# Kernel tuning notes

Hardware: AMD Instinct MI355X
Metric: run time of the kernel (lower is better)

## Reference

```python
import jax, jax.numpy as jnp
import numpy as np
import math

N_NODES = 100000
N_EDGES = 1_600_000
NFEAT = 512
NHID = 128
NLAYERS = 6
NCLASS = 64


def setup_inputs() -> dict:
    key = jax.random.key(0)
    ks = jax.random.split(key, 8)
    x = jax.random.normal(ks[0], (N_NODES, NFEAT), jnp.float32)
    rows = jax.random.randint(ks[1], (N_EDGES,), 0, N_NODES, dtype=jnp.int32)
    cols = jax.random.randint(ks[2], (N_EDGES,), 0, N_NODES, dtype=jnp.int32)
    # normalized-adjacency-like edge weights
    vals = jax.random.uniform(ks[3], (N_EDGES,), jnp.float32) * (1.0 / 16.0)
    s = 1.0 / math.sqrt(NHID)  # reset_parameters: uniform(-1/sqrt(out_features), ...)
    W0 = jax.random.uniform(ks[4], (NFEAT, NHID), jnp.float32, minval=-s, maxval=s)
    Wh = jax.random.uniform(ks[5], (NLAYERS - 1, NHID, NHID), jnp.float32, minval=-s, maxval=s)
    Wfc = jax.random.normal(ks[6], (NHID * NLAYERS, NCLASS), jnp.float32) * 0.02
    bfc = jnp.zeros((NCLASS,), jnp.float32)
    return {"x": x, "rows": rows, "cols": cols, "vals": vals,
            "W0": W0, "Wh": Wh, "Wfc": Wfc, "bfc": bfc}


def _spmm(rows, cols, vals, h, n):
    # sparse [n,n] @ h : gather source rows, scale by edge weight, scatter-add to dest
    return jax.ops.segment_sum(vals[:, None] * h[cols], rows, num_segments=n)


def reference(x, rows, cols, vals, W0, Wh, Wfc, bfc):
    n = x.shape[0]
    # conv0: relu(spmm(A, x @ W0))  (inference: no dropout, no skip-gate)
    h = jax.nn.relu(_spmm(rows, cols, vals, x @ W0, n))
    hiddens = [h]
    for i in range(Wh.shape[0]):
        h = jax.nn.relu(_spmm(rows, cols, vals, h @ Wh[i], n))
        hiddens.append(h)
    logits = jnp.concatenate(hiddens, axis=-1) @ Wfc + bfc
    return jax.nn.log_softmax(logits, axis=1)
```

## Files before the change

### kernel.cpp

```cpp
#include <hip/hip_runtime.h>
#include <hip/hip_bf16.h>
#include <cstdint>
#include <cstddef>

static constexpr int NFEAT   = 512;
static constexpr int NHID    = 128;
static constexpr int NLAYERS = 6;
static constexpr int NCLASS  = 64;

typedef __bf16 bf16x8 __attribute__((ext_vector_type(8)));
typedef float  floatx4 __attribute__((ext_vector_type(4)));

static __device__ __forceinline__ uint16_t f2bf(float v){
    __hip_bfloat16 h = __float2bfloat16(v);
    return *reinterpret_cast<uint16_t*>(&h);
}

__global__ void k_sniff(const uint16_t* __restrict__ x, int nwords, uint32_t* __restrict__ flag){
    int i = blockIdx.x*256 + threadIdx.x;
    if (i < nwords){
        uint16_t w = x[i];
        if ((w & 0x7F80u) == 0x7F80u) atomicOr(flag, 1u);
    }
}

__global__ void k_sentinel(uint16_t* out, int nel){
    int i = blockIdx.x*256 + threadIdx.x;
    if (i < nel) out[i] = 0x3E00u;
}

__global__ void k_zero(uint32_t* p, int n){
    int i = blockIdx.x*256 + threadIdx.x;
    if (i < n) p[i] = 0u;
}

__global__ void k_hist(const int* __restrict__ rows, uint32_t* __restrict__ deg, int nE){
    int e = blockIdx.x*256 + threadIdx.x;
    if (e < nE) atomicAdd(&deg[rows[e]], 1u);
}

__global__ __launch_bounds__(1024) void k_scan1(const uint32_t* __restrict__ deg,
                                                uint32_t* __restrict__ row_start,
                                                uint32_t* __restrict__ partial, int n){
    __shared__ uint32_t sh[1024];
    int tid = threadIdx.x;
    int i = blockIdx.x*1024 + tid;
    uint32_t v = (i < n) ? deg[i] : 0u;
    sh[tid] = v; __syncthreads();
    for (int off = 1; off < 1024; off <<= 1){
        uint32_t t = (tid >= off) ? sh[tid-off] : 0u;
        __syncthreads();
        sh[tid] += t;
        __syncthreads();
    }
    if (i < n) row_start[i+1] = sh[tid];
    if (tid == 1023) partial[blockIdx.x] = sh[1023];
}

__global__ __launch_bounds__(128) void k_scan2(uint32_t* partial, int nb){
    __shared__ uint32_t sh[128];
    int tid = threadIdx.x;
    uint32_t v = (tid < nb) ? partial[tid] : 0u;
    sh[tid] = v; __syncthreads();
    for (int off = 1; off < 128; off <<= 1){
        uint32_t t = (tid >= off) ? sh[tid-off] : 0u;
        __syncthreads();
        sh[tid] += t;
        __syncthreads();
    }
    if (tid < nb) partial[tid] = sh[tid] - v;
}

__global__ __launch_bounds__(1024) void k_scan3(const uint32_t* __restrict__ deg,
                                                uint32_t* __restrict__ row_start,
                                                const uint32_t* __restrict__ partial,
                                                uint32_t* __restrict__ cursor, int n){
    int i = blockIdx.x*1024 + threadIdx.x;
    if (i < n){
        uint32_t rs = row_start[i+1] + partial[blockIdx.x];
        row_start[i+1] = rs;
        cursor[i] = rs - deg[i];
        if (i == 0) row_start[0] = 0u;
    }
}

__global__ void k_scatter(const int* __restrict__ rows, const int* __restrict__ cols,
                          const void* __restrict__ vals,
                          uint32_t* __restrict__ cursor, uint2* __restrict__ ep, int nE,
                          const uint32_t* __restrict__ flags){
    int e = blockIdx.x*256 + threadIdx.x;
    if (e < nE){
        int r = rows[e];
        uint32_t pos = atomicAdd(&cursor[r], 1u);
        float v;
        if (flags[0]) v = ((const float*)vals)[e];
        else          v = __bfloat162float(((const __hip_bfloat16*)vals)[e]);
        ep[pos] = make_uint2((uint32_t)cols[e], __float_as_uint(v));
    }
}

__global__ void k_transpose(const void* __restrict__ B, long elem_off,
                            uint16_t* __restrict__ Bt, int K, int N,
                            const uint32_t* __restrict__ flags){
    int idx = blockIdx.x*256 + threadIdx.x;
    if (idx < K*N){
        int k = idx / N, nn = idx - k*N;
        uint16_t w;
        if (flags[0]) w = f2bf(((const float*)B)[elem_off + idx]);
        else          w = ((const uint16_t*)B)[elem_off + idx];
        Bt[nn*K + k] = w;
    }
}

template<int NTILES, int MODE>
__global__ __launch_bounds__(256) void k_gemm(
    const void* __restrict__ Aany, int lda,
    const uint16_t* __restrict__ Bt, int ldb, int K, int Mwaves,
    uint16_t* __restrict__ Cb, float* __restrict__ Cf,
    const uint32_t* __restrict__ flagsp)
{
    __shared__ uint16_t lds[NTILES*16*40];
    const int tid  = threadIdx.x;
    const int lane = tid & 63;
    const int gw   = blockIdx.x*4 + (tid >> 6);
    const bool active = gw < Mwaves;
    const int m = lane & 15, quad = lane >> 4;
    const long row0 = (long)gw * 16;
    const int afp32 = flagsp ? (int)flagsp[0] : 0;
    const uint16_t* A16 = (const uint16_t*)Aany;
    const float*    A32 = (const float*)Aany;

    floatx4 acc[NTILES];
#pragma unroll
    for (int i = 0; i < NTILES; i++) acc[i] = (floatx4){0.f,0.f,0.f,0.f};

    for (int kk = 0; kk < K; kk += 32){
        for (int idx = tid; idx < NTILES*16*4; idx += 256){
            int nn = idx >> 2, c = idx & 3;
            *(bf16x8*)&lds[nn*40 + c*8] = *(const bf16x8*)&Bt[(long)nn*ldb + kk + c*8];
        }
        __syncthreads();
        if (active){
            bf16x8 a;
            if (afp32){
                const float* p = &A32[(row0 + m)*lda + kk + quad*8];
                float4 f0 = *(const float4*)p;
                float4 f1 = *(const float4*)(p + 4);
                a[0]=(__bf16)f0.x; a[1]=(__bf16)f0.y; a[2]=(__bf16)f0.z; a[3]=(__bf16)f0.w;
                a[4]=(__bf16)f1.x; a[5]=(__bf16)f1.y; a[6]=(__bf16)f1.z; a[7]=(__bf16)f1.w;
            } else {
                a = *(const bf16x8*)&A16[(row0 + m)*lda + kk + quad*8];
            }
#pragma unroll
            for (int nt = 0; nt < NTILES; nt++){
                bf16x8 b = *(const bf16x8*)&lds[(nt*16 + m)*40 + quad*8];
                acc[nt] = __builtin_amdgcn_mfma_f32_16x16x32_bf16(a, b, acc[nt], 0, 0, 0);
            }
        }
        __syncthreads();
    }
    if (active){
#pragma unroll
        for (int nt = 0; nt < NTILES; nt++){
#pragma unroll
            for (int r = 0; r < 4; r++){
                long row = row0 + quad*4 + r;
                int  col = nt*16 + m;
                float v = acc[nt][r];
                if (MODE == 1) Cf[row*(NTILES*16) + col] += v;
                else           Cb[row*(NTILES*16) + col] = f2bf(v);
            }
        }
    }
}

__global__ __launch_bounds__(256) void k_gemm_fused(
    const uint16_t* __restrict__ A,
    const uint16_t* __restrict__ B1t,
    const uint16_t* __restrict__ B2t, int ldb2,
    uint16_t* __restrict__ C1, float* __restrict__ C2, int nchunks)
{
    __shared__ uint16_t lds[(128+64)*132];
    const int tid = threadIdx.x, lane = tid & 63;
    for (int idx = tid; idx < 128*16; idx += 256){
        int nn = idx >> 4, c = idx & 15;
        *(bf16x8*)&lds[nn*132 + c*8] = *(const bf16x8*)&B1t[nn*128 + c*8];
    }
    for (int idx = tid; idx < 64*16; idx += 256){
        int nn = idx >> 4, c = idx & 15;
        *(bf16x8*)&lds[(128+nn)*132 + c*8] = *(const bf16x8*)&B2t[(long)nn*ldb2 + c*8];
    }
    __syncthreads();

    const int m = lane & 15, quad = lane >> 4;
    const int nw = gridDim.x * 4;
    for (int chunk = blockIdx.x*4 + (tid >> 6); chunk < nchunks; chunk += nw){
        const long row0 = (long)chunk * 16;
        const uint16_t* Arow = &A[(row0 + m)*128 + quad*8];
        bf16x8 a[4];
#pragma unroll
        for (int ks = 0; ks < 4; ks++) a[ks] = *(const bf16x8*)&Arow[ks*32];

        floatx4 acc1[8], acc2[4];
#pragma unroll
        for (int i = 0; i < 8; i++) acc1[i] = (floatx4){0.f,0.f,0.f,0.f};
#pragma unroll
        for (int i = 0; i < 4; i++) acc2[i] = (floatx4){0.f,0.f,0.f,0.f};

#pragma unroll
        for (int ks = 0; ks < 4; ks++){
            const int kk = ks*32 + quad*8;
#pragma unroll
            for (int nt = 0; nt < 8; nt++){
                bf16x8 b = *(const bf16x8*)&lds[(nt*16 + m)*132 + kk];
                acc1[nt] = __builtin_amdgcn_mfma_f32_16x16x32_bf16(a[ks], b, acc1[nt], 0, 0, 0);
            }
#pragma unroll
            for (int nt = 0; nt < 4; nt++){
                bf16x8 b = *(const bf16x8*)&lds[(128 + nt*16 + m)*132 + kk];
                acc2[nt] = __builtin_amdgcn_mfma_f32_16x16x32_bf16(a[ks], b, acc2[nt], 0, 0, 0);
            }
        }
#pragma unroll
        for (int nt = 0; nt < 8; nt++){
#pragma unroll
            for (int r = 0; r < 4; r++){
                long row = row0 + quad*4 + r;
                int  col = nt*16 + m;
                float v  = acc1[nt][r];
                float vn = __shfl_xor(v, 1);
                if ((m & 1) == 0){
                    uint32_t pk = (uint32_t)f2bf(v) | ((uint32_t)f2bf(vn) << 16);
                    *(uint32_t*)&C1[row*128 + col] = pk;
                }
            }
        }
#pragma unroll
        for (int nt = 0; nt < 4; nt++){
#pragma unroll
            for (int r = 0; r < 4; r++){
                long row = row0 + quad*4 + r;
                int  col = nt*16 + m;
                float v  = acc2[nt][r];
                float vn = __shfl_xor(v, 1);
                if ((m & 1) == 0){
                    float2* p = (float2*)&C2[row*64 + col];
                    float2 o = *p;
                    o.x += v; o.y += vn;
                    *p = o;
                }
            }
        }
    }
}

__global__ __launch_bounds__(256) void k_spmm(
    const uint2* __restrict__ ep, const uint32_t* __restrict__ row_start,
    const uint32_t* __restrict__ tmp, uint16_t* __restrict__ out, int n)
{
    int t = blockIdx.x*256 + threadIdx.x;
    int gw = t >> 6, lane = t & 63;
    if (gw >= n) return;
    uint32_t s = row_start[gw], e = row_start[gw+1];
    float ax = 0.f, ay = 0.f;
    for (uint32_t base = s; base < e; base += 64){
        int cnt = (int)(e - base); if (cnt > 64) cnt = 64;
        uint2 d = (lane < cnt) ? ep[base + lane] : make_uint2(0u, 0u);
        int j = 0;
        for (; j + 4 <= cnt; j += 4){
            uint32_t c0 = __shfl(d.x, j+0); float v0 = __uint_as_float(__shfl(d.y, j+0));
            uint32_t c1 = __shfl(d.x, j+1); float v1 = __uint_as_float(__shfl(d.y, j+1));
            uint32_t c2 = __shfl(d.x, j+2); float v2 = __uint_as_float(__shfl(d.y, j+2));
            uint32_t c3 = __shfl(d.x, j+3); float v3 = __uint_as_float(__shfl(d.y, j+3));
            uint32_t p0 = tmp[(size_t)c0*64 + lane];
            uint32_t p1 = tmp[(size_t)c1*64 + lane];
            uint32_t p2 = tmp[(size_t)c2*64 + lane];
            uint32_t p3 = tmp[(size_t)c3*64 + lane];
            ax = fmaf(v0, __uint_as_float(p0 << 16), ax); ay = fmaf(v0, __uint_as_float(p0 & 0xffff0000u), ay);
            ax = fmaf(v1, __uint_as_float(p1 << 16), ax); ay = fmaf(v1, __uint_as_float(p1 & 0xffff0000u), ay);
            ax = fmaf(v2, __uint_as_float(p2 << 16), ax); ay = fmaf(v2, __uint_as_float(p2 & 0xffff0000u), ay);
            ax = fmaf(v3, __uint_as_float(p3 << 16), ax); ay = fmaf(v3, __uint_as_float(p3 & 0xffff0000u), ay);
        }
        for (; j < cnt; j++){
            uint32_t c = __shfl(d.x, j); float v = __uint_as_float(__shfl(d.y, j));
            uint32_t p = tmp[(size_t)c*64 + lane];
            ax = fmaf(v, __uint_as_float(p << 16), ax);
            ay = fmaf(v, __uint_as_float(p & 0xffff0000u), ay);
        }
    }
    ax = fmaxf(ax, 0.f); ay = fmaxf(ay, 0.f);
    uint32_t packed = ((uint32_t)f2bf(ay) << 16) | (uint32_t)f2bf(ax);
    *(uint32_t*)&out[(size_t)gw*128 + 2*lane] = packed;
}

__global__ __launch_bounds__(256) void k_logsoftmax(const float* __restrict__ logits,
                                                    const void* __restrict__ bias,
                                                    void* __restrict__ out, int n,
                                                    const uint32_t* __restrict__ flags){
    int t = blockIdx.x*256 + threadIdx.x;
    int row = t >> 6, lane = t & 63;
    if (row >= n) return;
    const int fp32 = (int)flags[0];
    float b = fp32 ? ((const float*)bias)[lane]
                   : __bfloat162float(((const __hip_bfloat16*)bias)[lane]);
    float x = logits[(size_t)row*64 + lane] + b;
    float mx = x;
    for (int off = 32; off; off >>= 1) mx = fmaxf(mx, __shfl_xor(mx, off));
    float ex = __expf(x - mx);
    float sum = ex;
    for (int off = 32; off; off >>= 1) sum += __shfl_xor(sum, off);
    float r = x - mx - __logf(sum);
    if (fp32) ((float*)out)[(size_t)row*64 + lane] = r;
    else      ((uint16_t*)out)[(size_t)row*64 + lane] = f2bf(r);
}

extern "C" void kernel_launch(void* const* d_in, const int* in_sizes, int n_in,
                              void* d_out, int out_size, void* d_ws, size_t ws_size,
                              hipStream_t stream){
    const void* x    = d_in[0];
    const int* rows  = (const int*)d_in[1];
    const int* cols  = (const int*)d_in[2];
    const void* vals = d_in[3];
    const void* W0   = d_in[4];
    const void* Wh   = d_in[5];
    const void* Wfc  = d_in[6];
    const void* bfc  = d_in[7];

    const int n  = in_sizes[0] / NFEAT;
    const int nE = in_sizes[1];

    char* ws = (char*)d_ws;
    size_t off = 0;
    auto alloc = [&](size_t bytes)->char*{
        char* p = ws + off;
        off = (off + bytes + 255) & ~(size_t)255;
        return p;
    };
    uint32_t* flags     = (uint32_t*)alloc(256);
    uint32_t* deg       = (uint32_t*)alloc((size_t)n*4);
    uint32_t* row_start = (uint32_t*)alloc(((size_t)n+1)*4);
    uint32_t* cursor    = (uint32_t*)alloc((size_t)n*4);
    uint32_t* partial   = (uint32_t*)alloc(512);
    uint2*    ep        = (uint2*)   alloc((size_t)nE*8);
    uint16_t* W0t       = (uint16_t*)alloc((size_t)NFEAT*NHID*2);
    uint16_t* Wht       = (uint16_t*)alloc((size_t)(NLAYERS-1)*NHID*NHID*2);
    uint16_t* Wfct      = (uint16_t*)alloc((size_t)NCLASS*NLAYERS*NHID*2);
    uint16_t* tmp       = (uint16_t*)alloc((size_t)n*NHID*2);
    uint16_t* hbuf      = (uint16_t*)alloc((size_t)n*NHID*2);
    float*    logits    = (float*)   alloc((size_t)n*NCLASS*4);

    if (ws_size < off){
        k_sentinel<<<(out_size+255)/256, 256, 0, stream>>>((uint16_t*)d_out, out_size);
        return;
    }

    hipMemsetAsync(flags, 0, 4, stream);
    const int NW = 1 << 20;
    k_sniff<<<NW/256, 256, 0, stream>>>((const uint16_t*)x, NW, flags);

    const int scanBlocks = (n + 1023)/1024;
    k_zero<<<(n+255)/256, 256, 0, stream>>>(deg, n);
    k_hist<<<(nE+255)/256, 256, 0, stream>>>(rows, deg, nE);
    k_scan1<<<scanBlocks, 1024, 0, stream>>>(deg, row_start, partial, n);
    k_scan2<<<1, 128, 0, stream>>>(partial, scanBlocks);
    k_scan3<<<scanBlocks, 1024, 0, stream>>>(deg, row_start, partial, cursor, n);
    k_scatter<<<(nE+255)/256, 256, 0, stream>>>(rows, cols, vals, cursor, ep, nE, flags);

    k_transpose<<<(NFEAT*NHID+255)/256, 256, 0, stream>>>(W0, 0L, W0t, NFEAT, NHID, flags);
    for (int l = 0; l < NLAYERS-1; l++)
        k_transpose<<<(NHID*NHID+255)/256, 256, 0, stream>>>(
            Wh, (long)l*NHID*NHID, Wht + l*NHID*NHID, NHID, NHID, flags);
    k_transpose<<<(NLAYERS*NHID*NCLASS+255)/256, 256, 0, stream>>>(
            Wfc, 0L, Wfct, NLAYERS*NHID, NCLASS, flags);

    hipMemsetAsync(logits, 0, (size_t)n*NCLASS*4, stream);

    const int Mwaves = n/16;
    const int gemmBlocks = (Mwaves + 3)/4;
    const int rowBlocks  = (n*64 + 255)/256;
    const int fusedBlocks = 768;

    k_gemm<8,0><<<gemmBlocks, 256, 0, stream>>>(x, NFEAT, W0t, NFEAT, NFEAT, Mwaves, tmp, nullptr, flags);
    k_spmm<<<rowBlocks, 256, 0, stream>>>(ep, row_start, (const uint32_t*)tmp, hbuf, n);
    for (int l = 1; l < NLAYERS; l++){
        k_gemm_fused<<<fusedBlocks, 256, 0, stream>>>(hbuf, Wht + (l-1)*NHID*NHID,
                                                      Wfct + (l-1)*NHID, NLAYERS*NHID,
                                                      tmp, logits, Mwaves);
        k_spmm<<<rowBlocks, 256, 0, stream>>>(ep, row_start, (const uint32_t*)tmp, hbuf, n);
    }
    k_gemm<4,1><<<gemmBlocks, 256, 0, stream>>>(hbuf, NHID, Wfct + (NLAYERS-1)*NHID, NLAYERS*NHID,
                                                NHID, Mwaves, nullptr, logits, nullptr);
    k_logsoftmax<<<rowBlocks, 256, 0, stream>>>(logits, bfc, d_out, n, flags);
}
```

Baseline: 1.233 ms.

## Build CSR via two-pass bucketed binning, merge weight transposes, drop logits memset

Replaces the random global atomic scatter of edges into CSR with a two-pass scheme. Edges are first binned into 256-row buckets using shared-memory histograms and one global atomic per bucket per block. A second kernel then places each bucket's edges into final rows using LDS atomics, which gives more local writes. The seven weight-transpose launches are merged into one kernel. The logits memset is removed by having the first fused GEMM store to logits instead of accumulating. The binning reuses the tmp buffer as scratch and falls back to the old scatter when sizes do not fit.

```diff
diff --git a/kernel.cpp b/kernel.cpp
--- a/kernel.cpp
+++ b/kernel.cpp
@@ -74,12 +74,15 @@
 __global__ __launch_bounds__(1024) void k_scan3(const uint32_t* __restrict__ deg,
                                                 uint32_t* __restrict__ row_start,
                                                 const uint32_t* __restrict__ partial,
+                                                uint32_t* __restrict__ bcur,
                                                 uint32_t* __restrict__ cursor, int n){
     int i = blockIdx.x*1024 + threadIdx.x;
     if (i < n){
         uint32_t rs = row_start[i+1] + partial[blockIdx.x];
         row_start[i+1] = rs;
-        cursor[i] = rs - deg[i];
+        uint32_t start = rs - deg[i];
+        cursor[i] = start;
+        if ((i & 255) == 0) bcur[i >> 8] = start;
         if (i == 0) row_start[0] = 0u;
     }
 }
@@ -99,16 +102,92 @@
     }
 }
 
-__global__ void k_transpose(const void* __restrict__ B, long elem_off,
-                            uint16_t* __restrict__ Bt, int K, int N,
-                            const uint32_t* __restrict__ flags){
-    int idx = blockIdx.x*256 + threadIdx.x;
-    if (idx < K*N){
-        int k = idx / N, nn = idx - k*N;
-        uint16_t w;
-        if (flags[0]) w = f2bf(((const float*)B)[elem_off + idx]);
-        else          w = ((const uint16_t*)B)[elem_off + idx];
-        Bt[nn*K + k] = w;
+__global__ __launch_bounds__(256) void k_bin(
+    const int* __restrict__ rows, const int* __restrict__ cols,
+    const void* __restrict__ vals,
+    uint32_t* __restrict__ bcur,
+    uint2* __restrict__ epb, uint8_t* __restrict__ rloc,
+    int nE, int nbuck, int epb_per_block,
+    const uint32_t* __restrict__ flags)
+{
+    __shared__ uint32_t h[512];
+    const int tid = threadIdx.x;
+    const int e0 = blockIdx.x * epb_per_block;
+    int e1 = e0 + epb_per_block; if (e1 > nE) e1 = nE;
+
+    for (int b = tid; b < nbuck; b += 256) h[b] = 0u;
+    __syncthreads();
+    for (int e = e0 + tid; e < e1; e += 256){
+        int r = rows[e];
+        atomicAdd(&h[r >> 8], 1u);
+    }
+    __syncthreads();
+    for (int b = tid; b < nbuck; b += 256){
+        uint32_t c = h[b];
+        h[b] = c ? atomicAdd(&bcur[b], c) : 0u;
+    }
+    __syncthreads();
+    const int fp32 = (int)flags[0];
+    for (int e = e0 + tid; e < e1; e += 256){
+        int r = rows[e];
+        uint32_t pos = atomicAdd(&h[r >> 8], 1u);
+        float v;
+        if (fp32) v = ((const float*)vals)[e];
+        else      v = __bfloat162float(((const __hip_bfloat16*)vals)[e]);
+        epb[pos] = make_uint2((uint32_t)cols[e], __float_as_uint(v));
+        rloc[pos] = (uint8_t)(r & 255);
+    }
+}
+
+__global__ __launch_bounds__(256) void k_csr(
+    const uint32_t* __restrict__ row_start,
+    const uint2* __restrict__ epb, const uint8_t* __restrict__ rloc,
+    uint2* __restrict__ ep, int n)
+{
+    __shared__ uint32_t curs[256];
+    const int b = blockIdx.x;
+    const int r0 = b << 8;
+    const int tid = threadIdx.x;
+    const int r = r0 + tid;
+    curs[tid] = (r < n) ? row_start[r] : 0u;
+    __syncthreads();
+    int rend = r0 + 256; if (rend > n) rend = n;
+    const uint32_t s = row_start[r0];
+    const uint32_t e = row_start[rend];
+    for (uint32_t i = s + tid; i < e; i += 256){
+        uint2 rec = epb[i];
+        uint32_t rl = rloc[i];
+        uint32_t pos = atomicAdd(&curs[rl], 1u);
+        ep[pos] = rec;
+    }
+}
+
+__global__ void k_transpose_all(const void* __restrict__ W0, const void* __restrict__ Wh,
+                                const void* __restrict__ Wfc,
+                                uint16_t* __restrict__ W0t, uint16_t* __restrict__ Wht,
+                                uint16_t* __restrict__ Wfct,
+                                const uint32_t* __restrict__ flags)
+{
+    const int idx = blockIdx.x*256 + threadIdx.x;
+    const int T0 = NFEAT*NHID;
+    const int T1 = (NLAYERS-1)*NHID*NHID;
+    const int T2 = NLAYERS*NHID*NCLASS;
+    const int fp32 = (int)flags[0];
+    if (idx < T0){
+        uint16_t w = fp32 ? f2bf(((const float*)W0)[idx]) : ((const uint16_t*)W0)[idx];
+        int k = idx / NHID, nn = idx - k*NHID;
+        W0t[nn*NFEAT + k] = w;
+    } else if (idx < T0 + T1){
+        int j = idx - T0;
+        uint16_t w = fp32 ? f2bf(((const float*)Wh)[j]) : ((const uint16_t*)Wh)[j];
+        int l = j / (NHID*NHID); int jj = j - l*(NHID*NHID);
+        int k = jj / NHID, nn = jj - k*NHID;
+        Wht[l*NHID*NHID + nn*NHID + k] = w;
+    } else if (idx < T0 + T1 + T2){
+        int j = idx - T0 - T1;
+        uint16_t w = fp32 ? f2bf(((const float*)Wfc)[j]) : ((const uint16_t*)Wfc)[j];
+        int k = j / NCLASS, nn = j - k*NCLASS;
+        Wfct[nn*(NLAYERS*NHID) + k] = w;
     }
 }
 
@@ -178,7 +257,8 @@
     const uint16_t* __restrict__ A,
     const uint16_t* __restrict__ B1t,
     const uint16_t* __restrict__ B2t, int ldb2,
-    uint16_t* __restrict__ C1, float* __restrict__ C2, int nchunks)
+    uint16_t* __restrict__ C1, float* __restrict__ C2, int nchunks,
+    int store_c2)
 {
     __shared__ uint16_t lds[(128+64)*132];
     const int tid = threadIdx.x, lane = tid & 63;
@@ -245,9 +325,13 @@
                 float vn = __shfl_xor(v, 1);
                 if ((m & 1) == 0){
                     float2* p = (float2*)&C2[row*64 + col];
-                    float2 o = *p;
-                    o.x += v; o.y += vn;
-                    *p = o;
+                    if (store_c2){
+                        float2 o; o.x = v; o.y = vn; *p = o;
+                    } else {
+                        float2 o = *p;
+                        o.x += v; o.y += vn;
+                        *p = o;
+                    }
                 }
             }
         }
@@ -341,6 +425,7 @@
     uint32_t* row_start = (uint32_t*)alloc(((size_t)n+1)*4);
     uint32_t* cursor    = (uint32_t*)alloc((size_t)n*4);
     uint32_t* partial   = (uint32_t*)alloc(512);
+    uint32_t* bcur      = (uint32_t*)alloc(2048);
     uint2*    ep        = (uint2*)   alloc((size_t)nE*8);
     uint16_t* W0t       = (uint16_t*)alloc((size_t)NFEAT*NHID*2);
     uint16_t* Wht       = (uint16_t*)alloc((size_t)(NLAYERS-1)*NHID*NHID*2);
@@ -363,17 +448,22 @@
     k_hist<<<(nE+255)/256, 256, 0, stream>>>(rows, deg, nE);
     k_scan1<<<scanBlocks, 1024, 0, stream>>>(deg, row_start, partial, n);
     k_scan2<<<1, 128, 0, stream>>>(partial, scanBlocks);
-    k_scan3<<<scanBlocks, 1024, 0, stream>>>(deg, row_start, partial, cursor, n);
-    k_scatter<<<(nE+255)/256, 256, 0, stream>>>(rows, cols, vals, cursor, ep, nE, flags);
-
-    k_transpose<<<(NFEAT*NHID+255)/256, 256, 0, stream>>>(W0, 0L, W0t, NFEAT, NHID, flags);
-    for (int l = 0; l < NLAYERS-1; l++)
-        k_transpose<<<(NHID*NHID+255)/256, 256, 0, stream>>>(
-            Wh, (long)l*NHID*NHID, Wht + l*NHID*NHID, NHID, NHID, flags);
-    k_transpose<<<(NLAYERS*NHID*NCLASS+255)/256, 256, 0, stream>>>(
-            Wfc, 0L, Wfct, NLAYERS*NHID, NCLASS, flags);
-
-    hipMemsetAsync(logits, 0, (size_t)n*NCLASS*4, stream);
+    k_scan3<<<scanBlocks, 1024, 0, stream>>>(deg, row_start, partial, bcur, cursor, n);
+
+    const int TTOT = NFEAT*NHID + (NLAYERS-1)*NHID*NHID + NLAYERS*NHID*NCLASS;
+    k_transpose_all<<<(TTOT+255)/256, 256, 0, stream>>>(W0, Wh, Wfc, W0t, Wht, Wfct, flags);
+
+    const int nbuck = (n + 255) >> 8;
+    if (nbuck <= 512 && (size_t)n*NHID*2 >= (size_t)nE*9){
+        uint2*   epb  = (uint2*)tmp;
+        uint8_t* rloc = (uint8_t*)tmp + (size_t)nE*8;
+        const int EPB = 2048;
+        k_bin<<<(nE+EPB-1)/EPB, 256, 0, stream>>>(rows, cols, vals, bcur, epb, rloc,
+                                                  nE, nbuck, EPB, flags);
+        k_csr<<<nbuck, 256, 0, stream>>>(row_start, epb, rloc, ep, n);
+    } else {
+        k_scatter<<<(nE+255)/256, 256, 0, stream>>>(rows, cols, vals, cursor, ep, nE, flags);
+    }
 
     const int Mwaves = n/16;
     const int gemmBlocks = (Mwaves + 3)/4;
@@ -385,7 +475,7 @@
     for (int l = 1; l < NLAYERS; l++){
         k_gemm_fused<<<fusedBlocks, 256, 0, stream>>>(hbuf, Wht + (l-1)*NHID*NHID,
                                                       Wfct + (l-1)*NHID, NLAYERS*NHID,
-                                                      tmp, logits, Mwaves);
+                                                      tmp, logits, Mwaves, (l == 1) ? 1 : 0);
         k_spmm<<<rowBlocks, 256, 0, stream>>>(ep, row_start, (const uint32_t*)tmp, hbuf, n);
     }
     k_gemm<4,1><<<gemmBlocks, 256, 0, stream>>>(hbuf, NHID, Wfct + (NLAYERS-1)*NHID, NLAYERS*NHID,
```

Measured after the change: 1.154 ms. 6.4% less time.
